# Kernel optimization log

Hardware: AMD Instinct MI355X
Metric: run time of the kernel (lower is better)

Reference implementation:

```python
import jax, jax.numpy as jnp
import numpy as np

N = 100000
E = 6400000


def _gcn_conv(x, edge_index, W, b, n_nodes):
    # Linear transform first (PyG GCNConv applies lin before propagate)
    h = x @ W  # [N, out]
    src = edge_index[0]
    dst = edge_index[1]
    # add self loops
    loop = jnp.arange(n_nodes, dtype=src.dtype)
    src = jnp.concatenate([src, loop])
    dst = jnp.concatenate([dst, loop])
    # symmetric normalization deg^-1/2 (deg computed on dst, incl. self loops)
    deg = jax.ops.segment_sum(jnp.ones(dst.shape, dtype=h.dtype), dst,
                              num_segments=n_nodes)
    dinv = jnp.where(deg > 0, jax.lax.rsqrt(deg), jnp.zeros_like(deg))
    norm = dinv[src] * dinv[dst]  # [E+N]
    # gather -> scale -> scatter-add
    msgs = h[src] * norm[:, None]  # [E+N, out]
    out = jax.ops.segment_sum(msgs, dst, num_segments=n_nodes)
    return out + b


def setup_inputs() -> dict:
    key = jax.random.key(0)
    k1, k2, k3, k4 = jax.random.split(key, 4)
    x = jax.random.normal(k1, (N, 1), dtype=jnp.float32)
    edge_index = jax.random.randint(k2, (2, E), 0, N, dtype=jnp.int64)
    # Glorot-ish init for weights, zero bias (PyG defaults)
    W1 = jax.random.normal(k3, (1, 32), dtype=jnp.float32) * (1.0 / np.sqrt(1.0))
    b1 = jnp.zeros((32,), dtype=jnp.float32)
    W2 = jax.random.normal(k4, (32, 2), dtype=jnp.float32) * (1.0 / np.sqrt(32.0))
    b2 = jnp.zeros((2,), dtype=jnp.float32)
    return {"x": x, "edge_index": edge_index, "W1": W1, "b1": b1,
            "W2": W2, "b2": b2}


def reference(x, edge_index, W1, b1, W2, b2):
    h = _gcn_conv(x, edge_index, W1, b1, N)
    h = jax.nn.relu(h)
    # dropout omitted: eval-mode (F.dropout is identity when not training)
    h = _gcn_conv(h, edge_index, W2, b2, N)
    return jax.nn.log_softmax(h, axis=1)
```

## Files before the change

kernel.cpp:

```cpp
#include <hip/hip_runtime.h>
#include <math.h>


#define NBK     13
#define BSHIFT  13
#define BSZ     8192
#define CAP     540672
#define R1REP   40
#define R2REP   20
#define ABLK    1024
#define BBLK    512
#define ACHUNK  8192


__global__ __launch_bounds__(BBLK) void bucketize_kernel(
        const int* __restrict__ src, const int* __restrict__ dst,
        unsigned* __restrict__ cursors, unsigned* __restrict__ ebuf, int E) {
    __shared__ unsigned stage[ACHUNK];
    __shared__ unsigned cnt[NBK], gbase[NBK], loff[NBK], run[NBK];
    int t = threadIdx.x;
    if (t < NBK) { cnt[t] = 0; run[t] = 0; }
    __syncthreads();
    int e0 = blockIdx.x * ACHUNK;
    unsigned pk[16];
    int bb[16];
#pragma unroll
    for (int k = 0; k < 4; ++k) {
        int be = e0 + k * (BBLK * 4) + t * 4;
        if (be + 4 <= E) {
            int4 s4 = *(const int4*)(src + be);
            int4 d4 = *(const int4*)(dst + be);
            pk[k*4+0] = ((unsigned)s4.x << BSHIFT) | ((unsigned)d4.x & (BSZ-1)); bb[k*4+0] = d4.x >> BSHIFT;
            pk[k*4+1] = ((unsigned)s4.y << BSHIFT) | ((unsigned)d4.y & (BSZ-1)); bb[k*4+1] = d4.y >> BSHIFT;
            pk[k*4+2] = ((unsigned)s4.z << BSHIFT) | ((unsigned)d4.z & (BSZ-1)); bb[k*4+2] = d4.z >> BSHIFT;
            pk[k*4+3] = ((unsigned)s4.w << BSHIFT) | ((unsigned)d4.w & (BSZ-1)); bb[k*4+3] = d4.w >> BSHIFT;
            atomicAdd(&cnt[bb[k*4+0]], 1u);
            atomicAdd(&cnt[bb[k*4+1]], 1u);
            atomicAdd(&cnt[bb[k*4+2]], 1u);
            atomicAdd(&cnt[bb[k*4+3]], 1u);
        } else {
#pragma unroll
            for (int j = 0; j < 4; ++j) {
                int e = be + j;
                if (e < E) {
                    int s = src[e], d = dst[e];
                    pk[k*4+j] = ((unsigned)s << BSHIFT) | ((unsigned)d & (BSZ-1));
                    bb[k*4+j] = d >> BSHIFT;
                    atomicAdd(&cnt[bb[k*4+j]], 1u);
                } else bb[k*4+j] = -1;
            }
        }
    }
    __syncthreads();
    if (t == 0) {
        unsigned acc = 0;
        for (int b = 0; b < NBK; ++b) { loff[b] = acc; acc += cnt[b]; }
    }
    __syncthreads();
    if (t < NBK && cnt[t] > 0) gbase[t] = atomicAdd(&cursors[t], cnt[t]);
#pragma unroll
    for (int k = 0; k < 16; ++k) {
        if (bb[k] >= 0) {
            unsigned p = loff[bb[k]] + atomicAdd(&run[bb[k]], 1u);
            stage[p] = pk[k];
        }
    }
    __syncthreads();
    for (int b = 0; b < NBK; ++b) {
        unsigned n = cnt[b], lo = loff[b], go = gbase[b];
        unsigned* dp = ebuf + (size_t)b * CAP;
        for (unsigned j = t; j < n; j += BBLK) {
            unsigned pos = go + j;
            if (pos < (unsigned)CAP) dp[pos] = stage[lo + j];
        }
    }
}

__global__ __launch_bounds__(ABLK) void b0_deg_kernel(
        const unsigned* __restrict__ ebuf, const unsigned* __restrict__ cursors,
        unsigned* __restrict__ part) {
    __shared__ unsigned acc[BSZ];
    int b = blockIdx.x / R1REP, r = blockIdx.x % R1REP;
    for (int j = threadIdx.x; j < BSZ; j += ABLK) acc[j] = 0;
    __syncthreads();
    unsigned c = cursors[b]; if (c > (unsigned)CAP) c = CAP;
    unsigned per = (((c + R1REP - 1) / R1REP) + 3u) & ~3u;
    unsigned i0 = r * per, i1 = i0 + per; if (i1 > c) i1 = c;
    const unsigned* eb = ebuf + (size_t)b * CAP;
    unsigned base = i0 + threadIdx.x * 4;
    for (; base + 4 <= i1; base += ABLK * 4) {
        uint4 pk = *(const uint4*)(eb + base);
        atomicAdd(&acc[pk.x & (BSZ-1)], 1u);
        atomicAdd(&acc[pk.y & (BSZ-1)], 1u);
        atomicAdd(&acc[pk.z & (BSZ-1)], 1u);
        atomicAdd(&acc[pk.w & (BSZ-1)], 1u);
    }
    if (base < i1) {
        for (unsigned i = base; i < i1; ++i) atomicAdd(&acc[eb[i] & (BSZ-1)], 1u);
    }
    __syncthreads();
    unsigned* p = part + (size_t)blockIdx.x * BSZ;
    for (int j = threadIdx.x; j < BSZ; j += ABLK) p[j] = acc[j];
}

__global__ void r0_kernel(const unsigned* __restrict__ part, const float* __restrict__ x,
                          float* __restrict__ dinv, float* __restrict__ xd, int N) {
    int i = blockIdx.x * blockDim.x + threadIdx.x;
    if (i >= N) return;
    int b = i >> BSHIFT, dl = i & (BSZ - 1);
    unsigned deg = 0;
    const unsigned* p = part + (size_t)(b * R1REP) * BSZ + dl;
#pragma unroll 8
    for (int r = 0; r < R1REP; ++r) deg += p[(size_t)r * BSZ];
    float di = rsqrtf((float)deg + 1.0f);
    dinv[i] = di;
    xd[i] = di * x[i];
}

__global__ __launch_bounds__(ABLK) void b1_agg1_kernel(
        const unsigned* __restrict__ ebuf, const unsigned* __restrict__ cursors,
        const float* __restrict__ xd, float* __restrict__ part) {
    __shared__ float acc[BSZ];
    int b = blockIdx.x / R1REP, r = blockIdx.x % R1REP;
    for (int j = threadIdx.x; j < BSZ; j += ABLK) acc[j] = 0.0f;
    __syncthreads();
    unsigned c = cursors[b]; if (c > (unsigned)CAP) c = CAP;
    unsigned per = (((c + R1REP - 1) / R1REP) + 3u) & ~3u;
    unsigned i0 = r * per, i1 = i0 + per; if (i1 > c) i1 = c;
    const unsigned* eb = ebuf + (size_t)b * CAP;
    unsigned base = i0 + threadIdx.x * 4;
    for (; base + 4 <= i1; base += ABLK * 4) {
        uint4 pk = *(const uint4*)(eb + base);
        float v0 = xd[pk.x >> BSHIFT];
        float v1 = xd[pk.y >> BSHIFT];
        float v2 = xd[pk.z >> BSHIFT];
        float v3 = xd[pk.w >> BSHIFT];
        atomicAdd(&acc[pk.x & (BSZ-1)], v0);
        atomicAdd(&acc[pk.y & (BSZ-1)], v1);
        atomicAdd(&acc[pk.z & (BSZ-1)], v2);
        atomicAdd(&acc[pk.w & (BSZ-1)], v3);
    }
    if (base < i1) {
        for (unsigned i = base; i < i1; ++i) {
            unsigned pk = eb[i];
            atomicAdd(&acc[pk & (BSZ-1)], xd[pk >> BSHIFT]);
        }
    }
    __syncthreads();
    float* p = part + (size_t)blockIdx.x * BSZ;
    for (int j = threadIdx.x; j < BSZ; j += ABLK) p[j] = acc[j];
}

__global__ void r1_kernel(const float* __restrict__ part, const float* __restrict__ x,
                          const float* __restrict__ dinv,
                          const float* __restrict__ W1, const float* __restrict__ b1,
                          const float* __restrict__ W2,
                          float2* __restrict__ ttp, float* __restrict__ os0,
                          float* __restrict__ os1, int N) {
    __shared__ float sW1[32], sb1[32], sW2[64];
    int t = threadIdx.x;
    if (t < 32) { sW1[t] = W1[t]; sb1[t] = b1[t]; }
    if (t < 64) sW2[t] = W2[t];
    __syncthreads();
    int i = blockIdx.x * blockDim.x + t;
    if (i >= N) return;
    int b = i >> BSHIFT, dl = i & (BSZ - 1);
    float S = 0.0f;
    const float* p = part + (size_t)(b * R1REP) * BSZ + dl;
#pragma unroll 8
    for (int r = 0; r < R1REP; ++r) S += p[(size_t)r * BSZ];
    float di = dinv[i];
    float s1v = di * di * x[i] + di * S;
    float a0 = 0.0f, a1 = 0.0f;
#pragma unroll
    for (int j = 0; j < 32; ++j) {
        float h = fmaxf(fmaf(s1v, sW1[j], sb1[j]), 0.0f);
        a0 = fmaf(h, sW2[2 * j], a0);
        a1 = fmaf(h, sW2[2 * j + 1], a1);
    }
    ttp[i] = make_float2(di * a0, di * a1);
    os0[i] = di * di * a0;
    os1[i] = di * di * a1;
}

__global__ __launch_bounds__(ABLK) void b2_agg2_kernel(
        const unsigned* __restrict__ ebuf, const unsigned* __restrict__ cursors,
        const float2* __restrict__ ttp, float* __restrict__ part) {
    __shared__ float a0[BSZ];
    __shared__ float a1[BSZ];
    int b = blockIdx.x / R2REP, r = blockIdx.x % R2REP;
    for (int j = threadIdx.x; j < BSZ; j += ABLK) { a0[j] = 0.0f; a1[j] = 0.0f; }
    __syncthreads();
    unsigned c = cursors[b]; if (c > (unsigned)CAP) c = CAP;
    unsigned per = (((c + R2REP - 1) / R2REP) + 3u) & ~3u;
    unsigned i0 = r * per, i1 = i0 + per; if (i1 > c) i1 = c;
    const unsigned* eb = ebuf + (size_t)b * CAP;
    unsigned base = i0 + threadIdx.x * 4;
    for (; base + 4 <= i1; base += ABLK * 4) {
        uint4 pk = *(const uint4*)(eb + base);
        float2 v0 = ttp[pk.x >> BSHIFT];
        float2 v1 = ttp[pk.y >> BSHIFT];
        float2 v2 = ttp[pk.z >> BSHIFT];
        float2 v3 = ttp[pk.w >> BSHIFT];
        atomicAdd(&a0[pk.x & (BSZ-1)], v0.x);
        atomicAdd(&a1[pk.x & (BSZ-1)], v0.y);
        atomicAdd(&a0[pk.y & (BSZ-1)], v1.x);
        atomicAdd(&a1[pk.y & (BSZ-1)], v1.y);
        atomicAdd(&a0[pk.z & (BSZ-1)], v2.x);
        atomicAdd(&a1[pk.z & (BSZ-1)], v2.y);
        atomicAdd(&a0[pk.w & (BSZ-1)], v3.x);
        atomicAdd(&a1[pk.w & (BSZ-1)], v3.y);
    }
    if (base < i1) {
        for (unsigned i = base; i < i1; ++i) {
            unsigned pk = eb[i];
            float2 v = ttp[pk >> BSHIFT];
            atomicAdd(&a0[pk & (BSZ-1)], v.x);
            atomicAdd(&a1[pk & (BSZ-1)], v.y);
        }
    }
    __syncthreads();
    float* p = part + (size_t)blockIdx.x * (2 * BSZ);
    for (int j = threadIdx.x; j < BSZ; j += ABLK) {
        p[j] = a0[j];
        p[BSZ + j] = a1[j];
    }
}

__global__ void r2_kernel(const float* __restrict__ part, const float* __restrict__ dinv,
                          const float* __restrict__ os0, const float* __restrict__ os1,
                          const float* __restrict__ b2v, float2* __restrict__ out, int N) {
    int i = blockIdx.x * blockDim.x + threadIdx.x;
    if (i >= N) return;
    int b = i >> BSHIFT, dl = i & (BSZ - 1);
    float S0 = 0.0f, S1 = 0.0f;
    const float* p = part + (size_t)(b * R2REP) * (2 * BSZ) + dl;
#pragma unroll 4
    for (int r = 0; r < R2REP; ++r) {
        S0 += p[(size_t)r * (2 * BSZ)];
        S1 += p[(size_t)r * (2 * BSZ) + BSZ];
    }
    float di = dinv[i];
    float z0 = di * S0 + os0[i] + b2v[0];
    float z1 = di * S1 + os1[i] + b2v[1];
    float m = fmaxf(z0, z1), mn = fminf(z0, z1);
    float l = m + logf(1.0f + __expf(mn - m));
    out[i] = make_float2(z0 - l, z1 - l);
}


__global__ void deg_kernel(const int* __restrict__ dst, float* __restrict__ deg, int E) {
    int e = blockIdx.x * blockDim.x + threadIdx.x;
    if (e < E) atomicAdd(&deg[dst[e]], 1.0f);
}

__global__ void dinv_kernel(const float* __restrict__ deg, const float* __restrict__ x,
                            float* __restrict__ dinv, float* __restrict__ s1, int N) {
    int i = blockIdx.x * blockDim.x + threadIdx.x;
    if (i < N) {
        float di = rsqrtf(deg[i] + 1.0f);
        dinv[i] = di;
        s1[i] = di * di * x[i];
    }
}

__global__ void agg1_kernel(const int* __restrict__ src, const int* __restrict__ dst,
                            const float* __restrict__ x, const float* __restrict__ dinv,
                            float* __restrict__ s1, int E) {
    int e = blockIdx.x * blockDim.x + threadIdx.x;
    if (e < E) {
        int s = src[e], d = dst[e];
        atomicAdd(&s1[d], dinv[s] * dinv[d] * x[s]);
    }
}

__global__ void node_mlp_kernel(const float* __restrict__ s1, const float* __restrict__ dinv,
                                const float* __restrict__ W1, const float* __restrict__ b1,
                                const float* __restrict__ W2,
                                float* __restrict__ t0, float* __restrict__ t1,
                                float* __restrict__ o0, float* __restrict__ o1, int N) {
    __shared__ float sW1[32], sb1[32], sW2[64];
    int t = threadIdx.x;
    if (t < 32) { sW1[t] = W1[t]; sb1[t] = b1[t]; }
    if (t < 64) sW2[t] = W2[t];
    __syncthreads();
    int i = blockIdx.x * blockDim.x + t;
    if (i < N) {
        float s = s1[i];
        float a0 = 0.0f, a1 = 0.0f;
#pragma unroll
        for (int j = 0; j < 32; ++j) {
            float h = fmaxf(fmaf(s, sW1[j], sb1[j]), 0.0f);
            a0 = fmaf(h, sW2[2 * j], a0);
            a1 = fmaf(h, sW2[2 * j + 1], a1);
        }
        t0[i] = a0; t1[i] = a1;
        float d2 = dinv[i] * dinv[i];
        o0[i] = d2 * a0; o1[i] = d2 * a1;
    }
}

__global__ void agg2_kernel(const int* __restrict__ src, const int* __restrict__ dst,
                            const float* __restrict__ dinv,
                            const float* __restrict__ t0, const float* __restrict__ t1,
                            float* __restrict__ o0, float* __restrict__ o1, int E) {
    int e = blockIdx.x * blockDim.x + threadIdx.x;
    if (e < E) {
        int s = src[e], d = dst[e];
        float w = dinv[s] * dinv[d];
        atomicAdd(&o0[d], w * t0[s]);
        atomicAdd(&o1[d], w * t1[s]);
    }
}

__global__ void logsoftmax_kernel(const float* __restrict__ o0, const float* __restrict__ o1,
                                  const float* __restrict__ b2, float* __restrict__ out, int N) {
    int i = blockIdx.x * blockDim.x + threadIdx.x;
    if (i < N) {
        float z0 = o0[i] + b2[0];
        float z1 = o1[i] + b2[1];
        float m = fmaxf(z0, z1), mn = fminf(z0, z1);
        float l = m + logf(1.0f + __expf(mn - m));
        ((float2*)out)[i] = make_float2(z0 - l, z1 - l);
    }
}


extern "C" void kernel_launch(void* const* d_in, const int* in_sizes, int n_in,
                              void* d_out, int out_size, void* d_ws, size_t ws_size,
                              hipStream_t stream) {
    const float* x  = (const float*)d_in[0];
    const int* ei   = (const int*)d_in[1];
    const float* W1 = (const float*)d_in[2];
    const float* b1 = (const float*)d_in[3];
    const float* W2 = (const float*)d_in[4];
    const float* b2 = (const float*)d_in[5];
    float* out = (float*)d_out;

    const int N = in_sizes[0];
    const int E = in_sizes[1] / 2;
    const int* src = ei;
    const int* dst = ei + E;

    const size_t OFF_CUR  = 0;
    const size_t OFF_EBUF = 256;
    const size_t SZ_EBUF  = (size_t)NBK * CAP * 4;
    const size_t OFF_PART = OFF_EBUF + SZ_EBUF;
    const size_t SZ_PART  = (size_t)NBK * R1REP * BSZ * 4;
    const size_t OFF_NODE = OFF_PART + SZ_PART;
    const size_t SZ_NODE  = (size_t)N * 4;
    const size_t NEED = OFF_NODE + 6 * SZ_NODE + 256;

    bool fast = (ws_size >= NEED) && (N <= NBK * BSZ) && (N < (1 << 17)) && N > 0 &&
                ((size_t)E * BSZ / (size_t)N + 16384 <= (size_t)CAP);

    if (fast) {
        unsigned* cursors = (unsigned*)((char*)d_ws + OFF_CUR);
        unsigned* ebuf    = (unsigned*)((char*)d_ws + OFF_EBUF);
        float*    part    = (float*)((char*)d_ws + OFF_PART);
        float*    dinv    = (float*)((char*)d_ws + OFF_NODE);
        float*    xd      = dinv + N;
        float*    os0     = xd + N;
        float*    os1     = os0 + N;
        float2*   ttp     = (float2*)(os1 + N);

        hipMemsetAsync(cursors, 0, 256, stream);

        int ablocks = (E + ACHUNK - 1) / ACHUNK;
        int ng = (N + 255) / 256;

        bucketize_kernel<<<ablocks, BBLK, 0, stream>>>(src, dst, cursors, ebuf, E);
        b0_deg_kernel<<<NBK * R1REP, ABLK, 0, stream>>>(ebuf, cursors, (unsigned*)part);
        r0_kernel<<<ng, 256, 0, stream>>>((unsigned*)part, x, dinv, xd, N);
        b1_agg1_kernel<<<NBK * R1REP, ABLK, 0, stream>>>(ebuf, cursors, xd, part);
        r1_kernel<<<ng, 256, 0, stream>>>(part, x, dinv, W1, b1, W2, ttp, os0, os1, N);
        b2_agg2_kernel<<<NBK * R2REP, ABLK, 0, stream>>>(ebuf, cursors, ttp, part);
        r2_kernel<<<ng, 256, 0, stream>>>(part, dinv, os0, os1, b2, (float2*)out, N);
    } else {
        float* deg  = (float*)d_ws;
        float* dinv = deg + N;
        float* s1   = dinv + N;
        float* t0   = s1 + N;
        float* t1   = t0 + N;
        float* o0   = t1 + N;
        float* o1   = o0 + N;

        hipMemsetAsync(deg, 0, (size_t)N * sizeof(float), stream);
        int eg = (E + 255) / 256, ng = (N + 255) / 256;
        deg_kernel<<<eg, 256, 0, stream>>>(dst, deg, E);
        dinv_kernel<<<ng, 256, 0, stream>>>(deg, x, dinv, s1, N);
        agg1_kernel<<<eg, 256, 0, stream>>>(src, dst, x, dinv, s1, E);
        node_mlp_kernel<<<ng, 256, 0, stream>>>(s1, dinv, W1, b1, W2, t0, t1, o0, o1, N);
        agg2_kernel<<<eg, 256, 0, stream>>>(src, dst, dinv, t0, t1, o0, o1, E);
        logsoftmax_kernel<<<ng, 256, 0, stream>>>(o0, o1, b2, out, N);
    }
}
```

Baseline: 255.6 us.

## Aggregate LDS atomics per wavefront, widen per-thread loads, use nontemporal memory ops

In the bucketize kernel, per-edge shared-memory atomics on the 13 bucket counters are replaced by wavefront ballots, so one leader lane issues one atomic per bucket group and the other lanes write at offsets computed from their rank. The aggregation kernels now use 512-thread blocks and have each thread load 16 packed edges with nontemporal loads, which puts more gathers in flight. Partial-sum and edge-buffer stores become nontemporal. The ballot loop over 13 buckets per element adds instruction overhead, and the smaller blocks may lower occupancy or per-block throughput.

```diff
diff --git a/kernel.cpp b/kernel.cpp
--- a/kernel.cpp
+++ b/kernel.cpp
@@ -8,9 +8,21 @@
 #define CAP     540672
 #define R1REP   40
 #define R2REP   20
-#define ABLK    1024
+#define ABLK    512
 #define BBLK    512
 #define ACHUNK  8192
+
+typedef unsigned uv4 __attribute__((ext_vector_type(4)));
+
+__device__ __forceinline__ uv4 ntload_u4(const unsigned* p) {
+    return __builtin_nontemporal_load((const uv4*)p);
+}
+__device__ __forceinline__ void ntstore_f(float* p, float v) {
+    __builtin_nontemporal_store(v, p);
+}
+__device__ __forceinline__ void ntstore_u(unsigned* p, unsigned v) {
+    __builtin_nontemporal_store(v, p);
+}
 
 
 __global__ __launch_bounds__(BBLK) void bucketize_kernel(
@@ -18,37 +30,49 @@
         unsigned* __restrict__ cursors, unsigned* __restrict__ ebuf, int E) {
     __shared__ unsigned stage[ACHUNK];
     __shared__ unsigned cnt[NBK], gbase[NBK], loff[NBK], run[NBK];
-    int t = threadIdx.x;
+    const int t = threadIdx.x;
+    const int lane = t & 63;
+    const unsigned long long lmask_lt = (1ull << lane) - 1ull;
     if (t < NBK) { cnt[t] = 0; run[t] = 0; }
     __syncthreads();
-    int e0 = blockIdx.x * ACHUNK;
+
+    const int e0 = blockIdx.x * ACHUNK;
     unsigned pk[16];
     int bb[16];
+    if (e0 + ACHUNK <= E) {
+        const int4* s4 = (const int4*)(src + e0) + t * 4;
+        const int4* d4 = (const int4*)(dst + e0) + t * 4;
 #pragma unroll
-    for (int k = 0; k < 4; ++k) {
-        int be = e0 + k * (BBLK * 4) + t * 4;
-        if (be + 4 <= E) {
-            int4 s4 = *(const int4*)(src + be);
-            int4 d4 = *(const int4*)(dst + be);
-            pk[k*4+0] = ((unsigned)s4.x << BSHIFT) | ((unsigned)d4.x & (BSZ-1)); bb[k*4+0] = d4.x >> BSHIFT;
-            pk[k*4+1] = ((unsigned)s4.y << BSHIFT) | ((unsigned)d4.y & (BSZ-1)); bb[k*4+1] = d4.y >> BSHIFT;
-            pk[k*4+2] = ((unsigned)s4.z << BSHIFT) | ((unsigned)d4.z & (BSZ-1)); bb[k*4+2] = d4.z >> BSHIFT;
-            pk[k*4+3] = ((unsigned)s4.w << BSHIFT) | ((unsigned)d4.w & (BSZ-1)); bb[k*4+3] = d4.w >> BSHIFT;
-            atomicAdd(&cnt[bb[k*4+0]], 1u);
-            atomicAdd(&cnt[bb[k*4+1]], 1u);
-            atomicAdd(&cnt[bb[k*4+2]], 1u);
-            atomicAdd(&cnt[bb[k*4+3]], 1u);
-        } else {
+        for (int k = 0; k < 4; ++k) {
+            int4 s = s4[k], d = d4[k];
+            pk[k*4+0] = ((unsigned)s.x << BSHIFT) | ((unsigned)d.x & (BSZ-1)); bb[k*4+0] = d.x >> BSHIFT;
+            pk[k*4+1] = ((unsigned)s.y << BSHIFT) | ((unsigned)d.y & (BSZ-1)); bb[k*4+1] = d.y >> BSHIFT;
+            pk[k*4+2] = ((unsigned)s.z << BSHIFT) | ((unsigned)d.z & (BSZ-1)); bb[k*4+2] = d.z >> BSHIFT;
+            pk[k*4+3] = ((unsigned)s.w << BSHIFT) | ((unsigned)d.w & (BSZ-1)); bb[k*4+3] = d.w >> BSHIFT;
+        }
+    } else {
 #pragma unroll
-            for (int j = 0; j < 4; ++j) {
-                int e = be + j;
-                if (e < E) {
-                    int s = src[e], d = dst[e];
-                    pk[k*4+j] = ((unsigned)s << BSHIFT) | ((unsigned)d & (BSZ-1));
-                    bb[k*4+j] = d >> BSHIFT;
-                    atomicAdd(&cnt[bb[k*4+j]], 1u);
-                } else bb[k*4+j] = -1;
-            }
+        for (int k = 0; k < 16; ++k) {
+            int e = e0 + t * 16 + k;
+            if (e < E) {
+                int s = src[e], d = dst[e];
+                pk[k] = ((unsigned)s << BSHIFT) | ((unsigned)d & (BSZ-1));
+                bb[k] = d >> BSHIFT;
+            } else bb[k] = -1;
+        }
+    }
+
+#pragma unroll 4
+    for (int k = 0; k < 16; ++k) {
+        int b = bb[k];
+        unsigned long long peers = 0;
+        for (int q = 0; q < NBK; ++q) {
+            unsigned long long m = __ballot(b == q);
+            if (b == q) peers = m;
+        }
+        if (b >= 0) {
+            int leader = __ffsll((long long)peers) - 1;
+            if (lane == leader) atomicAdd(&cnt[b], (unsigned)__popcll(peers));
         }
     }
     __syncthreads();
@@ -58,20 +82,30 @@
     }
     __syncthreads();
     if (t < NBK && cnt[t] > 0) gbase[t] = atomicAdd(&cursors[t], cnt[t]);
-#pragma unroll
+
+#pragma unroll 4
     for (int k = 0; k < 16; ++k) {
-        if (bb[k] >= 0) {
-            unsigned p = loff[bb[k]] + atomicAdd(&run[bb[k]], 1u);
-            stage[p] = pk[k];
-        }
-    }
-    __syncthreads();
+        int b = bb[k];
+        unsigned long long peers = 0;
+        for (int q = 0; q < NBK; ++q) {
+            unsigned long long m = __ballot(b == q);
+            if (b == q) peers = m;
+        }
+        int leader = (b >= 0) ? (__ffsll((long long)peers) - 1) : 0;
+        unsigned rank = (unsigned)__popcll(peers & lmask_lt);
+        unsigned wbase = 0;
+        if (b >= 0 && lane == leader) wbase = atomicAdd(&run[b], (unsigned)__popcll(peers));
+        wbase = (unsigned)__shfl((int)wbase, leader);
+        if (b >= 0) stage[loff[b] + wbase + rank] = pk[k];
+    }
+    __syncthreads();
+
     for (int b = 0; b < NBK; ++b) {
         unsigned n = cnt[b], lo = loff[b], go = gbase[b];
         unsigned* dp = ebuf + (size_t)b * CAP;
         for (unsigned j = t; j < n; j += BBLK) {
             unsigned pos = go + j;
-            if (pos < (unsigned)CAP) dp[pos] = stage[lo + j];
+            if (pos < (unsigned)CAP) ntstore_u(&dp[pos], stage[lo + j]);
         }
     }
 }
@@ -84,23 +118,28 @@
     for (int j = threadIdx.x; j < BSZ; j += ABLK) acc[j] = 0;
     __syncthreads();
     unsigned c = cursors[b]; if (c > (unsigned)CAP) c = CAP;
-    unsigned per = (((c + R1REP - 1) / R1REP) + 3u) & ~3u;
+    unsigned per = (((c + R1REP - 1) / R1REP) + 15u) & ~15u;
     unsigned i0 = r * per, i1 = i0 + per; if (i1 > c) i1 = c;
     const unsigned* eb = ebuf + (size_t)b * CAP;
-    unsigned base = i0 + threadIdx.x * 4;
-    for (; base + 4 <= i1; base += ABLK * 4) {
-        uint4 pk = *(const uint4*)(eb + base);
-        atomicAdd(&acc[pk.x & (BSZ-1)], 1u);
-        atomicAdd(&acc[pk.y & (BSZ-1)], 1u);
-        atomicAdd(&acc[pk.z & (BSZ-1)], 1u);
-        atomicAdd(&acc[pk.w & (BSZ-1)], 1u);
-    }
-    if (base < i1) {
-        for (unsigned i = base; i < i1; ++i) atomicAdd(&acc[eb[i] & (BSZ-1)], 1u);
-    }
+    unsigned base = i0 + threadIdx.x * 16;
+    for (; base + 16 <= i1; base += ABLK * 16) {
+        uv4 p0 = ntload_u4(eb + base);
+        uv4 p1 = ntload_u4(eb + base + 4);
+        uv4 p2 = ntload_u4(eb + base + 8);
+        uv4 p3 = ntload_u4(eb + base + 12);
+        atomicAdd(&acc[p0.x & (BSZ-1)], 1u); atomicAdd(&acc[p0.y & (BSZ-1)], 1u);
+        atomicAdd(&acc[p0.z & (BSZ-1)], 1u); atomicAdd(&acc[p0.w & (BSZ-1)], 1u);
+        atomicAdd(&acc[p1.x & (BSZ-1)], 1u); atomicAdd(&acc[p1.y & (BSZ-1)], 1u);
+        atomicAdd(&acc[p1.z & (BSZ-1)], 1u); atomicAdd(&acc[p1.w & (BSZ-1)], 1u);
+        atomicAdd(&acc[p2.x & (BSZ-1)], 1u); atomicAdd(&acc[p2.y & (BSZ-1)], 1u);
+        atomicAdd(&acc[p2.z & (BSZ-1)], 1u); atomicAdd(&acc[p2.w & (BSZ-1)], 1u);
+        atomicAdd(&acc[p3.x & (BSZ-1)], 1u); atomicAdd(&acc[p3.y & (BSZ-1)], 1u);
+        atomicAdd(&acc[p3.z & (BSZ-1)], 1u); atomicAdd(&acc[p3.w & (BSZ-1)], 1u);
+    }
+    for (unsigned i = base; i < i1; ++i) atomicAdd(&acc[eb[i] & (BSZ-1)], 1u);
     __syncthreads();
     unsigned* p = part + (size_t)blockIdx.x * BSZ;
-    for (int j = threadIdx.x; j < BSZ; j += ABLK) p[j] = acc[j];
+    for (int j = threadIdx.x; j < BSZ; j += ABLK) ntstore_u(&p[j], acc[j]);
 }
 
 __global__ void r0_kernel(const unsigned* __restrict__ part, const float* __restrict__ x,
@@ -125,30 +164,39 @@
     for (int j = threadIdx.x; j < BSZ; j += ABLK) acc[j] = 0.0f;
     __syncthreads();
     unsigned c = cursors[b]; if (c > (unsigned)CAP) c = CAP;
-    unsigned per = (((c + R1REP - 1) / R1REP) + 3u) & ~3u;
+    unsigned per = (((c + R1REP - 1) / R1REP) + 15u) & ~15u;
     unsigned i0 = r * per, i1 = i0 + per; if (i1 > c) i1 = c;
     const unsigned* eb = ebuf + (size_t)b * CAP;
-    unsigned base = i0 + threadIdx.x * 4;
-    for (; base + 4 <= i1; base += ABLK * 4) {
-        uint4 pk = *(const uint4*)(eb + base);
-        float v0 = xd[pk.x >> BSHIFT];
-        float v1 = xd[pk.y >> BSHIFT];
-        float v2 = xd[pk.z >> BSHIFT];
-        float v3 = xd[pk.w >> BSHIFT];
-        atomicAdd(&acc[pk.x & (BSZ-1)], v0);
-        atomicAdd(&acc[pk.y & (BSZ-1)], v1);
-        atomicAdd(&acc[pk.z & (BSZ-1)], v2);
-        atomicAdd(&acc[pk.w & (BSZ-1)], v3);
-    }
-    if (base < i1) {
-        for (unsigned i = base; i < i1; ++i) {
-            unsigned pk = eb[i];
-            atomicAdd(&acc[pk & (BSZ-1)], xd[pk >> BSHIFT]);
-        }
+    unsigned base = i0 + threadIdx.x * 16;
+    for (; base + 16 <= i1; base += ABLK * 16) {
+        uv4 p0 = ntload_u4(eb + base);
+        uv4 p1 = ntload_u4(eb + base + 4);
+        uv4 p2 = ntload_u4(eb + base + 8);
+        uv4 p3 = ntload_u4(eb + base + 12);
+        float v0  = xd[p0.x >> BSHIFT], v1  = xd[p0.y >> BSHIFT];
+        float v2  = xd[p0.z >> BSHIFT], v3  = xd[p0.w >> BSHIFT];
+        float v4  = xd[p1.x >> BSHIFT], v5  = xd[p1.y >> BSHIFT];
+        float v6  = xd[p1.z >> BSHIFT], v7  = xd[p1.w >> BSHIFT];
+        float v8  = xd[p2.x >> BSHIFT], v9  = xd[p2.y >> BSHIFT];
+        float v10 = xd[p2.z >> BSHIFT], v11 = xd[p2.w >> BSHIFT];
+        float v12 = xd[p3.x >> BSHIFT], v13 = xd[p3.y >> BSHIFT];
+        float v14 = xd[p3.z >> BSHIFT], v15 = xd[p3.w >> BSHIFT];
+        atomicAdd(&acc[p0.x & (BSZ-1)], v0);  atomicAdd(&acc[p0.y & (BSZ-1)], v1);
+        atomicAdd(&acc[p0.z & (BSZ-1)], v2);  atomicAdd(&acc[p0.w & (BSZ-1)], v3);
+        atomicAdd(&acc[p1.x & (BSZ-1)], v4);  atomicAdd(&acc[p1.y & (BSZ-1)], v5);
+        atomicAdd(&acc[p1.z & (BSZ-1)], v6);  atomicAdd(&acc[p1.w & (BSZ-1)], v7);
+        atomicAdd(&acc[p2.x & (BSZ-1)], v8);  atomicAdd(&acc[p2.y & (BSZ-1)], v9);
+        atomicAdd(&acc[p2.z & (BSZ-1)], v10); atomicAdd(&acc[p2.w & (BSZ-1)], v11);
+        atomicAdd(&acc[p3.x & (BSZ-1)], v12); atomicAdd(&acc[p3.y & (BSZ-1)], v13);
+        atomicAdd(&acc[p3.z & (BSZ-1)], v14); atomicAdd(&acc[p3.w & (BSZ-1)], v15);
+    }
+    for (unsigned i = base; i < i1; ++i) {
+        unsigned pk = eb[i];
+        atomicAdd(&acc[pk & (BSZ-1)], xd[pk >> BSHIFT]);
     }
     __syncthreads();
     float* p = part + (size_t)blockIdx.x * BSZ;
-    for (int j = threadIdx.x; j < BSZ; j += ABLK) p[j] = acc[j];
+    for (int j = threadIdx.x; j < BSZ; j += ABLK) ntstore_f(&p[j], acc[j]);
 }
 
 __global__ void r1_kernel(const float* __restrict__ part, const float* __restrict__ x,
@@ -192,38 +240,51 @@
     for (int j = threadIdx.x; j < BSZ; j += ABLK) { a0[j] = 0.0f; a1[j] = 0.0f; }
     __syncthreads();
     unsigned c = cursors[b]; if (c > (unsigned)CAP) c = CAP;
-    unsigned per = (((c + R2REP - 1) / R2REP) + 3u) & ~3u;
+    unsigned per = (((c + R2REP - 1) / R2REP) + 15u) & ~15u;
     unsigned i0 = r * per, i1 = i0 + per; if (i1 > c) i1 = c;
     const unsigned* eb = ebuf + (size_t)b * CAP;
-    unsigned base = i0 + threadIdx.x * 4;
-    for (; base + 4 <= i1; base += ABLK * 4) {
-        uint4 pk = *(const uint4*)(eb + base);
-        float2 v0 = ttp[pk.x >> BSHIFT];
-        float2 v1 = ttp[pk.y >> BSHIFT];
-        float2 v2 = ttp[pk.z >> BSHIFT];
-        float2 v3 = ttp[pk.w >> BSHIFT];
-        atomicAdd(&a0[pk.x & (BSZ-1)], v0.x);
-        atomicAdd(&a1[pk.x & (BSZ-1)], v0.y);
-        atomicAdd(&a0[pk.y & (BSZ-1)], v1.x);
-        atomicAdd(&a1[pk.y & (BSZ-1)], v1.y);
-        atomicAdd(&a0[pk.z & (BSZ-1)], v2.x);
-        atomicAdd(&a1[pk.z & (BSZ-1)], v2.y);
-        atomicAdd(&a0[pk.w & (BSZ-1)], v3.x);
-        atomicAdd(&a1[pk.w & (BSZ-1)], v3.y);
-    }
-    if (base < i1) {
-        for (unsigned i = base; i < i1; ++i) {
-            unsigned pk = eb[i];
-            float2 v = ttp[pk >> BSHIFT];
-            atomicAdd(&a0[pk & (BSZ-1)], v.x);
-            atomicAdd(&a1[pk & (BSZ-1)], v.y);
-        }
+    unsigned base = i0 + threadIdx.x * 16;
+    for (; base + 16 <= i1; base += ABLK * 16) {
+        uv4 p0 = ntload_u4(eb + base);
+        uv4 p1 = ntload_u4(eb + base + 4);
+        uv4 p2 = ntload_u4(eb + base + 8);
+        uv4 p3 = ntload_u4(eb + base + 12);
+        float2 v0  = ttp[p0.x >> BSHIFT], v1  = ttp[p0.y >> BSHIFT];
+        float2 v2  = ttp[p0.z >> BSHIFT], v3  = ttp[p0.w >> BSHIFT];
+        float2 v4  = ttp[p1.x >> BSHIFT], v5  = ttp[p1.y >> BSHIFT];
+        float2 v6  = ttp[p1.z >> BSHIFT], v7  = ttp[p1.w >> BSHIFT];
+        float2 v8  = ttp[p2.x >> BSHIFT], v9  = ttp[p2.y >> BSHIFT];
+        float2 v10 = ttp[p2.z >> BSHIFT], v11 = ttp[p2.w >> BSHIFT];
+        float2 v12 = ttp[p3.x >> BSHIFT], v13 = ttp[p3.y >> BSHIFT];
+        float2 v14 = ttp[p3.z >> BSHIFT], v15 = ttp[p3.w >> BSHIFT];
+        atomicAdd(&a0[p0.x & (BSZ-1)], v0.x);  atomicAdd(&a1[p0.x & (BSZ-1)], v0.y);
+        atomicAdd(&a0[p0.y & (BSZ-1)], v1.x);  atomicAdd(&a1[p0.y & (BSZ-1)], v1.y);
+        atomicAdd(&a0[p0.z & (BSZ-1)], v2.x);  atomicAdd(&a1[p0.z & (BSZ-1)], v2.y);
+        atomicAdd(&a0[p0.w & (BSZ-1)], v3.x);  atomicAdd(&a1[p0.w & (BSZ-1)], v3.y);
+        atomicAdd(&a0[p1.x & (BSZ-1)], v4.x);  atomicAdd(&a1[p1.x & (BSZ-1)], v4.y);
+        atomicAdd(&a0[p1.y & (BSZ-1)], v5.x);  atomicAdd(&a1[p1.y & (BSZ-1)], v5.y);
+        atomicAdd(&a0[p1.z & (BSZ-1)], v6.x);  atomicAdd(&a1[p1.z & (BSZ-1)], v6.y);
+        atomicAdd(&a0[p1.w & (BSZ-1)], v7.x);  atomicAdd(&a1[p1.w & (BSZ-1)], v7.y);
+        atomicAdd(&a0[p2.x & (BSZ-1)], v8.x);  atomicAdd(&a1[p2.x & (BSZ-1)], v8.y);
+        atomicAdd(&a0[p2.y & (BSZ-1)], v9.x);  atomicAdd(&a1[p2.y & (BSZ-1)], v9.y);
+        atomicAdd(&a0[p2.z & (BSZ-1)], v10.x); atomicAdd(&a1[p2.z & (BSZ-1)], v10.y);
+        atomicAdd(&a0[p2.w & (BSZ-1)], v11.x); atomicAdd(&a1[p2.w & (BSZ-1)], v11.y);
+        atomicAdd(&a0[p3.x & (BSZ-1)], v12.x); atomicAdd(&a1[p3.x & (BSZ-1)], v12.y);
+        atomicAdd(&a0[p3.y & (BSZ-1)], v13.x); atomicAdd(&a1[p3.y & (BSZ-1)], v13.y);
+        atomicAdd(&a0[p3.z & (BSZ-1)], v14.x); atomicAdd(&a1[p3.z & (BSZ-1)], v14.y);
+        atomicAdd(&a0[p3.w & (BSZ-1)], v15.x); atomicAdd(&a1[p3.w & (BSZ-1)], v15.y);
+    }
+    for (unsigned i = base; i < i1; ++i) {
+        unsigned pk = eb[i];
+        float2 v = ttp[pk >> BSHIFT];
+        atomicAdd(&a0[pk & (BSZ-1)], v.x);
+        atomicAdd(&a1[pk & (BSZ-1)], v.y);
     }
     __syncthreads();
     float* p = part + (size_t)blockIdx.x * (2 * BSZ);
     for (int j = threadIdx.x; j < BSZ; j += ABLK) {
-        p[j] = a0[j];
-        p[BSZ + j] = a1[j];
+        ntstore_f(&p[j], a0[j]);
+        ntstore_f(&p[BSZ + j], a1[j]);
     }
 }
 
@@ -364,7 +425,7 @@
         float*    os1     = os0 + N;
         float2*   ttp     = (float2*)(os1 + N);
 
-        hipMemsetAsync(cursors, 0, 256, stream);
+        (void)hipMemsetAsync(cursors, 0, 256, stream);
 
         int ablocks = (E + ACHUNK - 1) / ACHUNK;
         int ng = (N + 255) / 256;
@@ -385,7 +446,7 @@
         float* o0   = t1 + N;
         float* o1   = o0 + N;
 
-        hipMemsetAsync(deg, 0, (size_t)N * sizeof(float), stream);
+        (void)hipMemsetAsync(deg, 0, (size_t)N * sizeof(float), stream);
         int eg = (E + 255) / 256, ng = (N + 255) / 256;
         deg_kernel<<<eg, 256, 0, stream>>>(dst, deg, E);
         dinv_kernel<<<ng, 256, 0, stream>>>(deg, x, dinv, s1, N);
```

After: 287.4 us. +12.4%, slower.
